# Kernel optimization log

Measured on AMD Instinct MI355X. Metric: run time of the kernel, lower is better.

## Reference

```python
import jax, jax.numpy as jnp
import numpy as np

D_MODEL = 192
D_STATE = 64
D_CONV = 4
EXPAND = 2
HEADDIM = 64
CHUNK = 256
D_INNER = EXPAND * D_MODEL            # 384
NHEADS = D_INNER // HEADDIM           # 6
CONV_DIM = D_INNER + 2 * D_STATE      # 512 (ngroups=1)
D_IN_PROJ = 2 * D_INNER + 2 * D_STATE + NHEADS  # 902


def setup_inputs() -> dict:
    key = jax.random.key(0)
    ks = jax.random.split(key, 10)
    B, H, W = 8, 64, 64
    rn = lambda k, s, sc: jax.random.normal(k, s, jnp.float32) * sc
    return {
        "x": rn(ks[0], (B, D_MODEL, H, W), 1.0),
        "norm1_w": jnp.ones((D_MODEL,), jnp.float32),
        "norm1_b": jnp.zeros((D_MODEL,), jnp.float32),
        "in_proj_w": rn(ks[1], (D_IN_PROJ, D_MODEL), D_MODEL ** -0.5),
        "conv_w": rn(ks[2], (CONV_DIM, D_CONV), D_CONV ** -0.5),
        "conv_b": jnp.zeros((CONV_DIM,), jnp.float32),
        "dt_bias": jnp.log(jnp.expm1(jax.random.uniform(ks[3], (NHEADS,), jnp.float32, 0.001, 0.1))),
        "A_log": jnp.log(jax.random.uniform(ks[4], (NHEADS,), jnp.float32, 1.0, 16.0)),
        "D_skip": jnp.ones((NHEADS,), jnp.float32),
        "ssm_norm_w": jnp.ones((D_INNER,), jnp.float32),
        "out_proj_w": rn(ks[5], (D_MODEL, D_INNER), D_INNER ** -0.5),
        "norm2_w": jnp.ones((D_MODEL,), jnp.float32),
        "norm2_b": jnp.zeros((D_MODEL,), jnp.float32),
        "ffn_w1": rn(ks[6], (2 * D_MODEL, D_MODEL), D_MODEL ** -0.5),
        "ffn_b1": jnp.zeros((2 * D_MODEL,), jnp.float32),
        "ffn_w2": rn(ks[7], (D_MODEL, 2 * D_MODEL), (2 * D_MODEL) ** -0.5),
        "ffn_b2": jnp.zeros((D_MODEL,), jnp.float32),
    }


def _layernorm(x, w, b, eps=1e-5):
    mu = jnp.mean(x, -1, keepdims=True)
    var = jnp.mean((x - mu) ** 2, -1, keepdims=True)
    return (x - mu) * jax.lax.rsqrt(var + eps) * w + b


def _segsum(a):
    # a: (..., T) -> lower-triangular segment sums, -inf above diagonal
    T = a.shape[-1]
    cs = jnp.cumsum(a, -1)
    d = cs[..., :, None] - cs[..., None, :]
    mask = jnp.tril(jnp.ones((T, T), bool))
    return jnp.where(mask, d, -jnp.inf)


def _ssd(x, A, Bm, Cm):
    # chunked SSD (Mamba2 ssd_minimal). x:(b,l,h,p) pre-scaled by dt; A:(b,l,h)=dt*A_h; Bm,Cm:(b,l,h,n)
    b, l, h, p = x.shape
    c = l // CHUNK
    x = x.reshape(b, c, CHUNK, h, p)
    A = A.reshape(b, c, CHUNK, h).transpose(0, 3, 1, 2)          # (b,h,c,t)
    Bm = Bm.reshape(b, c, CHUNK, h, D_STATE)
    Cm = Cm.reshape(b, c, CHUNK, h, D_STATE)
    A_cs = jnp.cumsum(A, -1)                                      # (b,h,c,t)
    L = jnp.exp(_segsum(A))                                       # (b,h,c,t,t)
    Y_diag = jnp.einsum('bclhn,bcshn,bhcls,bcshp->bclhp', Cm, Bm, L, x)
    decay_states = jnp.exp(A_cs[..., -1:] - A_cs)                 # (b,h,c,t)
    states = jnp.einsum('bclhn,bhcl,bclhp->bchpn', Bm, decay_states, x)
    A_last = jnp.pad(A_cs[..., -1], ((0, 0), (0, 0), (1, 0)))     # (b,h,c+1)
    decay_chunk = jnp.exp(_segsum(A_last))                        # (b,h,c+1,c+1)
    states = jnp.concatenate([jnp.zeros_like(states[:, :1]), states], axis=1)
    new_states = jnp.einsum('bhzc,bchpn->bzhpn', decay_chunk, states)
    states = new_states[:, :-1]                                   # (b,c,h,p,n) inter-chunk init states
    Y_off = jnp.einsum('bclhn,bchpn,bhcl->bclhp', Cm, states, jnp.exp(A_cs))
    return (Y_diag + Y_off).reshape(b, l, h, p)


def _mamba2(u, in_proj_w, conv_w, conv_b, dt_bias, A_log, D_skip, ssm_norm_w, out_proj_w):
    # u: (b, L, d_model) -> (b, L, d_model)
    b, l, _ = u.shape
    zxbcdt = u @ in_proj_w.T                                      # (b,l,902)
    z = zxbcdt[..., :D_INNER]
    xBC = zxbcdt[..., D_INNER:D_INNER + CONV_DIM]
    dt = jax.nn.softplus(zxbcdt[..., -NHEADS:] + dt_bias)         # (b,l,h)
    # causal depthwise conv over sequence
    xBC_t = jax.lax.conv_general_dilated(
        xBC.transpose(0, 2, 1), conv_w[:, None, :], (1,), [(D_CONV - 1, 0)],
        feature_group_count=CONV_DIM, dimension_numbers=('NCH', 'OIH', 'NCH'))
    xBC = jax.nn.silu(xBC_t.transpose(0, 2, 1) + conv_b)
    xs = xBC[..., :D_INNER].reshape(b, l, NHEADS, HEADDIM)
    Bm = jnp.broadcast_to(xBC[..., D_INNER:D_INNER + D_STATE][:, :, None, :], (b, l, NHEADS, D_STATE))
    Cm = jnp.broadcast_to(xBC[..., D_INNER + D_STATE:][:, :, None, :], (b, l, NHEADS, D_STATE))
    A = -jnp.exp(A_log)                                           # (h,)
    y = _ssd(xs * dt[..., None], dt * A, Bm, Cm)
    y = y + xs * D_skip[None, None, :, None]
    y = y.reshape(b, l, D_INNER)
    g = y * jax.nn.silu(z)                                        # gated RMSNorm
    g = g * jax.lax.rsqrt(jnp.mean(g * g, -1, keepdims=True) + 1e-5) * ssm_norm_w
    return g @ out_proj_w.T


def reference(x, norm1_w, norm1_b, in_proj_w, conv_w, conv_b, dt_bias, A_log, D_skip,
              ssm_norm_w, out_proj_w, norm2_w, norm2_b, ffn_w1, ffn_b1, ffn_w2, ffn_b2):
    B, C, H, W = x.shape
    x_flat = x.transpose(0, 2, 3, 1).reshape(B, H * W, C)
    h1 = _layernorm(x_flat, norm1_w, norm1_b)
    # faithful to source: raw reshape (B,HW,C)->(B,C,H,W), then mixer flattens to (B,L,C)
    u = h1.reshape(B, C, H, W).reshape(B, C, H * W).transpose(0, 2, 1)
    m = _mamba2(u, in_proj_w, conv_w, conv_b, dt_bias, A_log, D_skip, ssm_norm_w, out_proj_w)
    m_flat = m.transpose(0, 2, 1).reshape(B, C, H, W).transpose(0, 2, 3, 1).reshape(B, H * W, C)
    x_flat = x_flat + m_flat
    h2 = _layernorm(x_flat, norm2_w, norm2_b)
    f = jax.nn.gelu(h2 @ ffn_w1.T + ffn_b1, approximate=False) @ ffn_w2.T + ffn_b2
    x_flat = x_flat + f
    return x_flat.reshape(B, H, W, C).transpose(0, 3, 1, 2)
```

## Files before the change

### kernel.cpp

```cpp
#include <hip/hip_runtime.h>
#include <hip/hip_bf16.h>

#define BATCH 8
#define CHN   192
#define LEN   4096
#define DI    384
#define NHEAD 6
#define DST   64
#define NCHK  16

typedef __attribute__((ext_vector_type(8))) short short8;
typedef __attribute__((ext_vector_type(4))) short short4v;
typedef __attribute__((ext_vector_type(4))) float f32x4;

__device__ __forceinline__ short f2b(float f) {
  unsigned u = __builtin_bit_cast(unsigned, f);
  unsigned r = (u + 0x7FFFu + ((u >> 16) & 1u)) >> 16;
  return (short)r;
}
__device__ __forceinline__ float bf2f(short s) {
  unsigned u = ((unsigned)(unsigned short)s) << 16;
  return __builtin_bit_cast(float, u);
}

__global__ __launch_bounds__(256) void k_ln1(const float* __restrict__ x,
    const float* __restrict__ w, const float* __restrict__ b, float* __restrict__ h1) {
  __shared__ float s[192][33];
  __shared__ float red[2][32][8];
  __shared__ float mu_s[32], rs_s[32];
  int bb = blockIdx.y;
  int t0 = blockIdx.x * 32;
  int tid = threadIdx.x;
  for (int i = 0; i < 24; ++i) {
    int idx = tid + i * 256;
    int c = idx >> 5, tt = idx & 31;
    s[c][tt] = x[((size_t)bb * CHN + c) * LEN + t0 + tt];
  }
  __syncthreads();
  int tok = tid & 31, part = tid >> 5;
  float sum = 0.f, sq = 0.f;
  for (int c = part * 24; c < part * 24 + 24; ++c) { float v = s[c][tok]; sum += v; sq += v * v; }
  red[0][tok][part] = sum; red[1][tok][part] = sq;
  __syncthreads();
  if (tid < 32) {
    float su = 0.f, qq = 0.f;
    for (int p = 0; p < 8; ++p) { su += red[0][tid][p]; qq += red[1][tid][p]; }
    float mu = su / 192.f;
    float var = qq / 192.f - mu * mu;
    mu_s[tid] = mu; rs_s[tid] = rsqrtf(var + 1e-5f);
  }
  __syncthreads();
  for (int i = 0; i < 24; ++i) {
    int idx = tid + i * 256;
    int c = idx % 192, tt = idx / 192;
    float v = (s[c][tt] - mu_s[tt]) * rs_s[tt] * w[c] + b[c];
    h1[((size_t)bb * LEN + t0 + tt) * CHN + c] = v;
  }
}

__global__ void k_make_u(const float* __restrict__ h1, short* __restrict__ Ub) {
  __shared__ float s[32][33];
  int bb = blockIdx.z;
  int c0 = blockIdx.y * 32;
  int l0 = blockIdx.x * 32;
  int tx = threadIdx.x, ty = threadIdx.y;
  const float* src = h1 + (size_t)bb * (CHN * LEN);
  for (int i = 0; i < 4; ++i)
    s[ty + i * 8][tx] = src[(size_t)(c0 + ty + i * 8) * LEN + l0 + tx];
  __syncthreads();
  short* dstb = Ub + (size_t)bb * (CHN * LEN);
  for (int i = 0; i < 4; ++i)
    dstb[(size_t)(l0 + ty + i * 8) * CHN + c0 + tx] = f2b(s[tx][ty + i * 8]);
}

template <int EPI, int ABF16, int OBF16>
__global__ __launch_bounds__(256) void gemm_mfma(const void* __restrict__ Av,
    const float* __restrict__ W, const float* __restrict__ bias,
    void* __restrict__ Cv, int M, int N, int K, int ldc,
    const float* __restrict__ resid, float* __restrict__ outT) {
  __shared__ short Al[128 * 64];
  __shared__ short Wl[64 * 64];
  int m0 = blockIdx.y * 128, n0 = blockIdx.x * 64;
  int tid = threadIdx.x;
  int lane = tid & 63, wv = tid >> 6;
  int wm = (wv >> 1) * 64, wn = (wv & 1) * 32;
  int l15 = lane & 15, l4 = lane >> 4;
  f32x4 acc[4][2] = {};

  int ra = tid >> 1, ca = (tid & 1) * 32;
  int rw = tid >> 2, cw = (tid & 3) * 16;
  char* ArowL = (char*)Al + ra * 128;
  char* WrowL = (char*)Wl + rw * 128;
  int rxa = (ra & 7) << 4, rxw = (rw & 7) << 4;

  for (int k0 = 0; k0 < K; k0 += 64) {
    if (ABF16) {
      const short* Ag = (const short*)Av + (size_t)(m0 + ra) * K + k0 + ca;
#pragma unroll
      for (int q = 0; q < 4; ++q) {
        short8 pk = *(const short8*)(Ag + q * 8);
        *(short8*)(ArowL + (((ca + q * 8) * 2) ^ rxa)) = pk;
      }
    } else {
      const float* Ag = (const float*)Av + (size_t)(m0 + ra) * K + k0 + ca;
#pragma unroll
      for (int q = 0; q < 4; ++q) {
        float4 v0 = *(const float4*)(Ag + q * 8);
        float4 v1 = *(const float4*)(Ag + q * 8 + 4);
        short8 pk;
        pk[0] = f2b(v0.x); pk[1] = f2b(v0.y); pk[2] = f2b(v0.z); pk[3] = f2b(v0.w);
        pk[4] = f2b(v1.x); pk[5] = f2b(v1.y); pk[6] = f2b(v1.z); pk[7] = f2b(v1.w);
        *(short8*)(ArowL + (((ca + q * 8) * 2) ^ rxa)) = pk;
      }
    }
    {
      const float* Wg = W + (size_t)(n0 + rw) * K + k0 + cw;
#pragma unroll
      for (int q = 0; q < 2; ++q) {
        float4 v0 = *(const float4*)(Wg + q * 8);
        float4 v1 = *(const float4*)(Wg + q * 8 + 4);
        short8 pk;
        pk[0] = f2b(v0.x); pk[1] = f2b(v0.y); pk[2] = f2b(v0.z); pk[3] = f2b(v0.w);
        pk[4] = f2b(v1.x); pk[5] = f2b(v1.y); pk[6] = f2b(v1.z); pk[7] = f2b(v1.w);
        *(short8*)(WrowL + (((cw + q * 8) * 2) ^ rxw)) = pk;
      }
    }
    __syncthreads();
#pragma unroll
    for (int ks = 0; ks < 64; ks += 32) {
      short8 af[4], wf[2];
#pragma unroll
      for (int mf = 0; mf < 4; ++mf) {
        int rr = wm + mf * 16 + l15;
        af[mf] = *(const short8*)((const char*)Al + rr * 128 +
                                  (((ks + l4 * 8) * 2) ^ ((rr & 7) << 4)));
      }
#pragma unroll
      for (int nf = 0; nf < 2; ++nf) {
        int rr = wn + nf * 16 + l15;
        wf[nf] = *(const short8*)((const char*)Wl + rr * 128 +
                                  (((ks + l4 * 8) * 2) ^ ((rr & 7) << 4)));
      }
#pragma unroll
      for (int mf = 0; mf < 4; ++mf)
#pragma unroll
        for (int nf = 0; nf < 2; ++nf)
          acc[mf][nf] = __builtin_amdgcn_mfma_f32_16x16x32_bf16(
              af[mf], wf[nf], acc[mf][nf], 0, 0, 0);
    }
    __syncthreads();
  }
#pragma unroll
  for (int mf = 0; mf < 4; ++mf) {
#pragma unroll
    for (int nf = 0; nf < 2; ++nf) {
      int col = n0 + wn + nf * 16 + l15;
      float bv = (EPI >= 1 && EPI <= 3) ? bias[col] : 0.f;
      if (EPI == 3) {
        int row0 = m0 + wm + mf * 16 + l4 * 4;
        float4 o;
#pragma unroll
        for (int reg = 0; reg < 4; ++reg) {
          int row = row0 + reg;
          ((float*)&o)[reg] = acc[mf][nf][reg] + bv + resid[(size_t)row * CHN + col];
        }
        int bb_l = row0 >> 12, row_l = row0 & 4095;
        *(float4*)&outT[((size_t)bb_l * CHN + col) * LEN + row_l] = o;
      } else if (EPI == 4) {
        int row0 = m0 + wm + mf * 16 + l4 * 4;
        int bb_l = row0 >> 12, row_l = row0 & 4095;
        float4 xv = *(const float4*)&resid[((size_t)bb_l * CHN + col) * LEN + row_l];
#pragma unroll
        for (int reg = 0; reg < 4; ++reg)
          ((float*)Cv)[(size_t)(row0 + reg) * ldc + col] =
              acc[mf][nf][reg] + ((const float*)&xv)[reg];
      } else {
#pragma unroll
        for (int reg = 0; reg < 4; ++reg) {
          int row = m0 + wm + mf * 16 + l4 * 4 + reg;
          float v = acc[mf][nf][reg];
          if (EPI >= 1) v += bv;
          if (EPI == 1) v = 0.5f * v * (1.f + erff(v * 0.70710678118f));
          if (OBF16) ((short*)Cv)[(size_t)row * ldc + col] = f2b(v);
          else       ((float*)Cv)[(size_t)row * ldc + col] = v;
        }
      }
    }
  }
}

__global__ __launch_bounds__(256) void k_dt2(const float* __restrict__ h1,
    const float* __restrict__ win, const float* __restrict__ dt_bias,
    float* __restrict__ dtb) {
  __shared__ float Ut[192][65];
  __shared__ float Wl[6][192];
  int l0 = blockIdx.x * 64, bb = blockIdx.y;
  int tid = threadIdx.x;
  for (int i = tid; i < 6 * 192; i += 256)
    Wl[i / 192][i % 192] = win[(size_t)(896 + i / 192) * 192 + (i % 192)];
  const float* src = h1 + (size_t)bb * (CHN * LEN);
  for (int i = tid; i < 192 * 16; i += 256) {
    int c = i >> 4, q = i & 15;
    float4 v = *(const float4*)&src[(size_t)c * LEN + l0 + q * 4];
    *(float4*)&Ut[c][q * 4] = v;
  }
  __syncthreads();
  int tok = tid & 63, grp = tid >> 6;
  for (int h = grp; h < 6; h += 4) {
    float acc = dt_bias[h];
    for (int c = 0; c < 192; ++c) acc += Ut[c][tok] * Wl[h][c];
    dtb[((size_t)bb * LEN + l0 + tok) * NHEAD + h] =
        (acc > 20.f) ? acc : log1pf(expf(acc));
  }
}

__global__ __launch_bounds__(256) void k_conv(const short* __restrict__ zxs,
    const float* __restrict__ cw, const float* __restrict__ cb,
    short* __restrict__ xbcs) {
  __shared__ float S[67][132];
  int l0 = blockIdx.x * 64, ct = blockIdx.y, bb = blockIdx.z;
  int tid = threadIdx.x;
  int c = (tid & 31) * 4;
  int chb = ct * 128 + c;
  float wr[4][4];
#pragma unroll
  for (int j = 0; j < 4; ++j) {
    float4 w4 = *(const float4*)&cw[(size_t)(chb + j) * 4];
    wr[j][0] = w4.x; wr[j][1] = w4.y; wr[j][2] = w4.z; wr[j][3] = w4.w;
  }
  float4 bc4 = *(const float4*)&cb[chb];
  for (int idx = tid; idx < 67 * 16; idx += 256) {
    int r = idx >> 4, c8 = (idx & 15) * 8;
    int tok = l0 + r - 3;
    if (tok >= 0) {
      short8 v = *(const short8*)&zxs[((size_t)bb * LEN + tok) * 896 + 384 + ct * 128 + c8];
#pragma unroll
      for (int j = 0; j < 8; ++j) S[r][c8 + j] = bf2f(v[j]);
    } else {
#pragma unroll
      for (int j = 0; j < 8; ++j) S[r][c8 + j] = 0.f;
    }
  }
  __syncthreads();
  int t0l = tid >> 5;
#pragma unroll
  for (int it = 0; it < 8; ++it) {
    int tl = it * 8 + t0l;
    float a0 = bc4.x, a1 = bc4.y, a2 = bc4.z, a3 = bc4.w;
#pragma unroll
    for (int k = 0; k < 4; ++k) {
      float4 v = *(const float4*)&S[tl + k][c];
      a0 += v.x * wr[0][k];
      a1 += v.y * wr[1][k];
      a2 += v.z * wr[2][k];
      a3 += v.w * wr[3][k];
    }
    short4v o;
    o[0] = f2b(a0 / (1.f + __expf(-a0)));
    o[1] = f2b(a1 / (1.f + __expf(-a1)));
    o[2] = f2b(a2 / (1.f + __expf(-a2)));
    o[3] = f2b(a3 / (1.f + __expf(-a3)));
    *(short4v*)&xbcs[((size_t)bb * LEN + l0 + tl) * 512 + chb] = o;
  }
}

__global__ __launch_bounds__(256) void k_cumsum(const float* __restrict__ dtb,
    const float* __restrict__ A_log, float* __restrict__ sAg) {
  int cch = blockIdx.x, bb = blockIdx.y;
  int lane = threadIdx.x & 63, wv = threadIdx.x >> 6;
  size_t rowbase = (size_t)bb * LEN + cch * 256;
  for (int h = wv; h < NHEAD; h += 4) {
    float Ah = -expf(A_log[h]);
    float v[4];
#pragma unroll
    for (int i = 0; i < 4; ++i)
      v[i] = dtb[(rowbase + lane * 4 + i) * NHEAD + h] * Ah;
    v[1] += v[0]; v[2] += v[1]; v[3] += v[2];
    float tot = v[3];
    float sc = tot;
    for (int off = 1; off < 64; off <<= 1) {
      float o = __shfl_up(sc, off);
      if (lane >= off) sc += o;
    }
    float excl = sc - tot;
#pragma unroll
    for (int i = 0; i < 4; ++i)
      sAg[(rowbase + lane * 4 + i) * NHEAD + h] = v[i] + excl;
  }
}

__global__ __launch_bounds__(256) void k_xt(const short* __restrict__ xbcs,
    const float* __restrict__ dtb, const float* __restrict__ sAg,
    short* __restrict__ XT, short* __restrict__ XE, short* __restrict__ BtG) {
  int cch = blockIdx.x, h = blockIdx.y, bb = blockIdx.z;
  int tid = threadIdx.x;
  __shared__ float sD[256], sEl[256];
  __shared__ float T[64][68];
  size_t rowbase = (size_t)bb * LEN + cch * 256;
  sD[tid] = dtb[(rowbase + tid) * NHEAD + h];
  {
    float a = sAg[(rowbase + tid) * NHEAD + h];
    float atot = sAg[(rowbase + 255) * NHEAD + h];
    sEl[tid] = __expf(atot - a);
  }
  size_t base_xh = (((size_t)bb * NHEAD + h) * NCHK + cch) * 16384;
  size_t base_bc = ((size_t)bb * NCHK + cch) * 16384;
  int r = tid >> 2, cq = (tid & 3) * 16;
  int p = tid >> 2, sq = tid & 3;
  for (int ts = 0; ts < 4; ++ts) {
    __syncthreads();
#pragma unroll
    for (int q = 0; q < 2; ++q) {
      short8 v = *(const short8*)&xbcs[(rowbase + ts * 64 + r) * 512 + h * 64 + cq + q * 8];
#pragma unroll
      for (int j = 0; j < 8; ++j) T[r][cq + q * 8 + j] = bf2f(v[j]);
    }
    __syncthreads();
    {
      short8 x0, x1, e0, e1;
#pragma unroll
      for (int j = 0; j < 8; ++j) {
        int sl = sq * 16 + j;
        float f = T[sl][p] * sD[ts * 64 + sl];
        x0[j] = f2b(f);
        e0[j] = f2b(f * sEl[ts * 64 + sl]);
      }
#pragma unroll
      for (int j = 0; j < 8; ++j) {
        int sl = sq * 16 + 8 + j;
        float f = T[sl][p] * sD[ts * 64 + sl];
        x1[j] = f2b(f);
        e1[j] = f2b(f * sEl[ts * 64 + sl]);
      }
      size_t o = base_xh + (size_t)p * 256 + ts * 64 + sq * 16;
      *(short8*)&XT[o] = x0; *(short8*)&XT[o + 8] = x1;
      *(short8*)&XE[o] = e0; *(short8*)&XE[o + 8] = e1;
    }
    if (h == 0) {
      __syncthreads();
#pragma unroll
      for (int q = 0; q < 2; ++q) {
        short8 bv = *(const short8*)&xbcs[(rowbase + ts * 64 + r) * 512 + 384 + cq + q * 8];
#pragma unroll
        for (int j = 0; j < 8; ++j) T[r][cq + q * 8 + j] = bf2f(bv[j]);
      }
      __syncthreads();
      short8 b0, b1;
#pragma unroll
      for (int j = 0; j < 8; ++j) b0[j] = f2b(T[sq * 16 + j][p]);
#pragma unroll
      for (int j = 0; j < 8; ++j) b1[j] = f2b(T[sq * 16 + 8 + j][p]);
      size_t o = base_bc + (size_t)p * 256 + ts * 64 + sq * 16;
      *(short8*)&BtG[o] = b0; *(short8*)&BtG[o + 8] = b1;
    }
  }
}

__global__ __launch_bounds__(256) void k_states(const short* __restrict__ XE,
    const short* __restrict__ BtG, float* __restrict__ states) {
  int cch = blockIdx.x, h = blockIdx.y, bb = blockIdx.z;
  int tid = threadIdx.x;
  int lane = tid & 63, wv = tid >> 6;
  int l15 = lane & 15, l4 = lane >> 4;
  size_t base_bc = ((size_t)bb * NCHK + cch) * 16384;
  size_t base_xh = (((size_t)bb * NHEAD + h) * NCHK + cch) * 16384;
  f32x4 stacc[4] = {};
#pragma unroll
  for (int ks = 0; ks < 8; ++ks) {
    short8 aE = *(const short8*)&XE[base_xh +
        (size_t)(wv * 16 + l15) * 256 + ks * 32 + l4 * 8];
#pragma unroll
    for (int ni = 0; ni < 4; ++ni) {
      short8 bB = *(const short8*)&BtG[base_bc +
          (size_t)(ni * 16 + l15) * 256 + ks * 32 + l4 * 8];
      stacc[ni] = __builtin_amdgcn_mfma_f32_16x16x32_bf16(aE, bB, stacc[ni], 0, 0, 0);
    }
  }
  size_t stbase = (((size_t)bb * NCHK + cch) * NHEAD + h) * 4096;
#pragma unroll
  for (int ni = 0; ni < 4; ++ni)
#pragma unroll
    for (int reg = 0; reg < 4; ++reg)
      states[stbase + (size_t)(wv * 16 + l4 * 4 + reg) * 64 + ni * 16 + l15] =
          stacc[ni][reg];
}

__global__ void k_scan(const float* __restrict__ states, const float* __restrict__ sAg,
                       short* __restrict__ SinB) {
  int h = blockIdx.x, bb = blockIdx.y;
  int t = threadIdx.x;
  float S[16];
#pragma unroll
  for (int i = 0; i < 16; ++i) S[i] = 0.f;
  for (int z = 0; z < NCHK; ++z) {
    size_t base = (((size_t)bb * NCHK + z) * NHEAD + h) * 4096 + t * 16;
#pragma unroll
    for (int i = 0; i < 16; ++i) SinB[base + i] = f2b(S[i]);
    float az = __expf(sAg[((size_t)bb * LEN + z * 256 + 255) * NHEAD + h]);
#pragma unroll
    for (int i = 0; i < 16; ++i) S[i] = S[i] * az + states[base + i];
  }
}

__global__ __launch_bounds__(256) void k_ssdY(const short* __restrict__ xbcs,
    const short* __restrict__ XT, const short* __restrict__ SinB,
    const float* __restrict__ sAg, short* __restrict__ ybs) {
  int cch = blockIdx.x, h = blockIdx.y, bb = blockIdx.z;
  int tid = threadIdx.x;
  int lane = tid & 63, wv = tid >> 6;
  int l15 = lane & 15, l4 = lane >> 4;
  __shared__ float sA[256];
  __shared__ float sEt[256];
  __shared__ short St[4][64 * 64];
  size_t rowbase = (size_t)bb * LEN + cch * 256;
  {
    float av = sAg[(rowbase + tid) * NHEAD + h];
    sA[tid] = av;
    sEt[tid] = __expf(av);
  }
  __syncthreads();
  size_t base_xh = (((size_t)bb * NHEAD + h) * NCHK + cch) * 16384;
  size_t base_s = (((size_t)bb * NCHK + cch) * NHEAD + h) * 4096;
  int tp = wv;
  short* Sw = St[wv];
  short8 cf[4][2];
#pragma unroll
  for (int ni = 0; ni < 4; ++ni)
#pragma unroll
    for (int ks = 0; ks < 2; ++ks)
      cf[ni][ks] = *(const short8*)&xbcs[(rowbase + tp * 64 + ni * 16 + l15) * 512 +
                                         448 + ks * 32 + l4 * 8];
  float At[4];
#pragma unroll
  for (int ni = 0; ni < 4; ++ni) At[ni] = sA[tp * 64 + ni * 16 + l15];

  f32x4 yacc[4][4];
#pragma unroll
  for (int mi = 0; mi < 4; ++mi) {
    f32x4 yo[4] = {};
#pragma unroll
    for (int ks = 0; ks < 2; ++ks) {
      short8 aS = *(const short8*)&SinB[base_s +
          (size_t)(mi * 16 + l15) * 64 + ks * 32 + l4 * 8];
#pragma unroll
      for (int ni = 0; ni < 4; ++ni)
        yo[ni] = __builtin_amdgcn_mfma_f32_16x16x32_bf16(aS, cf[ni][ks], yo[ni], 0, 0, 0);
    }
#pragma unroll
    for (int ni = 0; ni < 4; ++ni) {
      float et = sEt[tp * 64 + ni * 16 + l15];
#pragma unroll
      for (int reg = 0; reg < 4; ++reg) yacc[mi][ni][reg] = et * yo[ni][reg];
    }
  }
  for (int st = 0; st <= tp; ++st) {
    bool diag = (st == tp);
#pragma unroll
    for (int mi = 0; mi < 4; ++mi) {
      const short* brow = &xbcs[(rowbase + st * 64 + mi * 16 + l15) * 512 + 384 + l4 * 8];
      short8 af0 = *(const short8*)brow;
      short8 af1 = *(const short8*)(brow + 32);
      f32x4 s0[4];
#pragma unroll
      for (int ni = 0; ni < 4; ++ni) {
        f32x4 t = {};
        t = __builtin_amdgcn_mfma_f32_16x16x32_bf16(af0, cf[ni][0], t, 0, 0, 0);
        t = __builtin_amdgcn_mfma_f32_16x16x32_bf16(af1, cf[ni][1], t, 0, 0, 0);
        s0[ni] = t;
      }
      float As[4];
#pragma unroll
      for (int reg = 0; reg < 4; ++reg) As[reg] = sA[st * 64 + mi * 16 + l4 * 4 + reg];
      int s_loc0 = mi * 16 + l4 * 4;
#pragma unroll
      for (int ni = 0; ni < 4; ++ni) {
        int t_loc = ni * 16 + l15;
        short4v pk;
#pragma unroll
        for (int reg = 0; reg < 4; ++reg) {
          float v = __expf(At[ni] - As[reg]) * s0[ni][reg];
          if (diag && (s_loc0 + reg) > t_loc) v = 0.f;
          pk[reg] = f2b(v);
        }
        *(short4v*)((char*)Sw + t_loc * 128 +
                    (((s_loc0 * 2)) ^ ((t_loc & 7) << 4))) = pk;
      }
    }
#pragma unroll
    for (int ks = 0; ks < 2; ++ks) {
      short8 bS[4], aX[4];
#pragma unroll
      for (int ni = 0; ni < 4; ++ni) {
        int rt = ni * 16 + l15;
        bS[ni] = *(const short8*)((const char*)Sw + rt * 128 +
                                  (((ks * 32 + l4 * 8) * 2) ^ ((rt & 7) << 4)));
      }
#pragma unroll
      for (int mi = 0; mi < 4; ++mi)
        aX[mi] = *(const short8*)&XT[base_xh +
            (size_t)(mi * 16 + l15) * 256 + st * 64 + ks * 32 + l4 * 8];
#pragma unroll
      for (int mi = 0; mi < 4; ++mi)
#pragma unroll
        for (int ni = 0; ni < 4; ++ni)
          yacc[mi][ni] = __builtin_amdgcn_mfma_f32_16x16x32_bf16(
              aX[mi], bS[ni], yacc[mi][ni], 0, 0, 0);
    }
  }
#pragma unroll
  for (int ni = 0; ni < 4; ++ni) {
    int tg = tp * 64 + ni * 16 + l15;
#pragma unroll
    for (int mi = 0; mi < 4; ++mi) {
      short4v o;
#pragma unroll
      for (int reg = 0; reg < 4; ++reg) o[reg] = f2b(yacc[mi][ni][reg]);
      *(short4v*)&ybs[(rowbase + tg) * DI + h * 64 + mi * 16 + l4 * 4] = o;
    }
  }
}

__global__ __launch_bounds__(128) void k_gate(const short* __restrict__ ybs,
    const short* __restrict__ zxs, const short* __restrict__ xbcs,
    const float* __restrict__ Dsk, const float* __restrict__ nw,
    short* __restrict__ gn) {
  int row = blockIdx.x;
  int tid = threadIdx.x;
  float g[3]; float sq = 0.f;
#pragma unroll
  for (int i = 0; i < 3; ++i) {
    int d = tid + i * 128;
    int h = d >> 6;
    float z = bf2f(zxs[(size_t)row * 896 + d]);
    float yy = bf2f(ybs[(size_t)row * DI + d]) +
               Dsk[h] * bf2f(xbcs[(size_t)row * 512 + d]);
    float gg = yy * (z / (1.f + expf(-z)));
    g[i] = gg; sq += gg * gg;
  }
  for (int off = 32; off > 0; off >>= 1) sq += __shfl_down(sq, off);
  __shared__ float wsum[2];
  if ((tid & 63) == 0) wsum[tid >> 6] = sq;
  __syncthreads();
  float rs = rsqrtf((wsum[0] + wsum[1]) / 384.f + 1e-5f);
#pragma unroll
  for (int i = 0; i < 3; ++i) {
    int d = tid + i * 128;
    gn[(size_t)row * DI + d] = f2b(g[i] * rs * nw[d]);
  }
}

__global__ __launch_bounds__(64) void k_ln2(const float* __restrict__ r,
    const float* __restrict__ w, const float* __restrict__ b, short* __restrict__ h2) {
  int row = blockIdx.x;
  int tid = threadIdx.x;
  float v[3]; float sum = 0.f;
#pragma unroll
  for (int i = 0; i < 3; ++i) { v[i] = r[(size_t)row * CHN + tid + i * 64]; sum += v[i]; }
  for (int off = 32; off > 0; off >>= 1) sum += __shfl_down(sum, off);
  sum = __shfl(sum, 0);
  float mu = sum / 192.f;
  float sq = 0.f;
#pragma unroll
  for (int i = 0; i < 3; ++i) { float d = v[i] - mu; sq += d * d; }
  for (int off = 32; off > 0; off >>= 1) sq += __shfl_down(sq, off);
  sq = __shfl(sq, 0);
  float rs = rsqrtf(sq / 192.f + 1e-5f);
#pragma unroll
  for (int i = 0; i < 3; ++i) {
    int c = tid + i * 64;
    h2[(size_t)row * CHN + c] = f2b((v[i] - mu) * rs * w[c] + b[c]);
  }
}

extern "C" void kernel_launch(void* const* d_in, const int* in_sizes, int n_in,
                              void* d_out, int out_size, void* d_ws, size_t ws_size,
                              hipStream_t stream) {
  const float* x     = (const float*)d_in[0];
  const float* n1w   = (const float*)d_in[1];
  const float* n1b   = (const float*)d_in[2];
  const float* win   = (const float*)d_in[3];
  const float* cw    = (const float*)d_in[4];
  const float* cb    = (const float*)d_in[5];
  const float* dtbw  = (const float*)d_in[6];
  const float* alog  = (const float*)d_in[7];
  const float* dskip = (const float*)d_in[8];
  const float* snw   = (const float*)d_in[9];
  const float* wout  = (const float*)d_in[10];
  const float* n2w   = (const float*)d_in[11];
  const float* n2b   = (const float*)d_in[12];
  const float* w1    = (const float*)d_in[13];
  const float* b1    = (const float*)d_in[14];
  const float* w2    = (const float*)d_in[15];
  const float* b2    = (const float*)d_in[16];
  float* out = (float*)d_out;

  int g = 8;
  size_t G192, S_ZXH, S_DT, S_XBCH, S_ST;
  for (;;) {
    G192   = (size_t)g * LEN * CHN;
    S_ZXH  = (size_t)g * LEN * 448;
    S_DT   = (size_t)g * LEN * NHEAD;
    S_XBCH = (size_t)g * LEN * 256;
    S_ST   = (size_t)g * NCHK * NHEAD * 4096;
    size_t TOTAL = 2 * G192 + S_ZXH + 2 * S_DT + S_XBCH + G192 / 2 +
                   2 * G192 + (size_t)g * 131072 + S_ST + S_ST / 2 + 64;
    if (TOTAL * 4 <= ws_size) break;
    if (g == 1) return;
    g >>= 1;
  }

  float* ws   = (float*)d_ws;
  float* h1   = ws;
  short* ybs  = (short*)ws;
  short* zxs  = (short*)(ws + 2 * G192);
  float* dtb  = ws + 2 * G192 + S_ZXH;
  float* sag  = dtb + S_DT;
  float* xbp  = sag + S_DT;
  short* xbcs = (short*)xbp;
  short* f1s  = (short*)xbp;
  float* up   = xbp + S_XBCH;
  short* Ubf  = (short*)up;
  short* h2s  = (short*)up;
  float* xtp  = up + G192 / 2;
  short* XT   = (short*)xtp;
  short* gns  = (short*)xtp;
  float* xep  = xtp + G192;
  short* XE   = (short*)xep;
  float* resid= xep;
  float* btp  = xep + G192;
  short* BtG  = (short*)btp;
  float* st   = btp + (size_t)g * 131072;
  short* SinB = (short*)(st + S_ST);

  const int M = g * LEN;

  for (int b0 = 0; b0 < BATCH; b0 += g) {
    const float* xg  = x   + (size_t)b0 * CHN * LEN;
    float*       og  = out + (size_t)b0 * CHN * LEN;

    k_ln1<<<dim3(LEN / 32, g), 256, 0, stream>>>(xg, n1w, n1b, h1);
    k_make_u<<<dim3(LEN / 32, CHN / 32, g), dim3(32, 8), 0, stream>>>(h1, Ubf);
    gemm_mfma<0, 1, 1><<<dim3(896 / 64, M / 128), 256, 0, stream>>>(
        Ubf, win, nullptr, zxs, M, 896, CHN, 896, nullptr, nullptr);
    k_dt2<<<dim3(LEN / 64, g), 256, 0, stream>>>(h1, win, dtbw, dtb);
    k_conv<<<dim3(LEN / 64, 4, g), 256, 0, stream>>>(zxs, cw, cb, xbcs);
    k_cumsum<<<dim3(NCHK, g), 256, 0, stream>>>(dtb, alog, sag);
    k_xt<<<dim3(NCHK, NHEAD, g), 256, 0, stream>>>(xbcs, dtb, sag, XT, XE, BtG);
    k_states<<<dim3(NCHK, NHEAD, g), 256, 0, stream>>>(XE, BtG, st);
    k_scan<<<dim3(NHEAD, g), 256, 0, stream>>>(st, sag, SinB);
    k_ssdY<<<dim3(NCHK, NHEAD, g), 256, 0, stream>>>(xbcs, XT, SinB, sag, ybs);
    k_gate<<<dim3(M), 128, 0, stream>>>(ybs, zxs, xbcs, dskip, snw, gns);
    gemm_mfma<4, 1, 0><<<dim3(CHN / 64, M / 128), 256, 0, stream>>>(
        gns, wout, nullptr, resid, M, CHN, DI, CHN, xg, nullptr);
    k_ln2<<<dim3(M), 64, 0, stream>>>(resid, n2w, n2b, h2s);
    gemm_mfma<1, 1, 1><<<dim3(DI / 64, M / 128), 256, 0, stream>>>(
        h2s, w1, b1, f1s, M, DI, CHN, DI, nullptr, nullptr);
    gemm_mfma<3, 1, 0><<<dim3(CHN / 64, M / 128), 256, 0, stream>>>(
        f1s, w2, b2, nullptr, M, CHN, DI, CHN, resid, og);
  }
}
```

Before: 269.1 us.

## Split SSD output kernel into one-wavefront blocks per 64-row subchunk

The intra-chunk SSD output kernel used 256-thread blocks where each wavefront handled one 64-row subchunk, with a causal triangle making wave work uneven (1 to 4 inner iterations). Now each block is a single wavefront covering one subchunk, launched on a grid four times larger, so finished waves release resources right away instead of waiting for the slowest wave in the block. The exp of the cumulative decay is computed in registers instead of being staged in shared memory. In exchange, every block reloads the full 256-entry decay vector, and there are more small blocks to schedule.

```diff
diff --git a/kernel.cpp b/kernel.cpp
--- a/kernel.cpp
+++ b/kernel.cpp
@@ -402,27 +402,21 @@
   }
 }
 
-__global__ __launch_bounds__(256) void k_ssdY(const short* __restrict__ xbcs,
+__global__ __launch_bounds__(64) void k_ssdY(const short* __restrict__ xbcs,
     const short* __restrict__ XT, const short* __restrict__ SinB,
     const float* __restrict__ sAg, short* __restrict__ ybs) {
-  int cch = blockIdx.x, h = blockIdx.y, bb = blockIdx.z;
-  int tid = threadIdx.x;
-  int lane = tid & 63, wv = tid >> 6;
+  int q = blockIdx.x;
+  int cch = q >> 2, tp = q & 3;
+  int h = blockIdx.y, bb = blockIdx.z;
+  int lane = threadIdx.x;
   int l15 = lane & 15, l4 = lane >> 4;
   __shared__ float sA[256];
-  __shared__ float sEt[256];
-  __shared__ short St[4][64 * 64];
+  __shared__ short St[64 * 64];
   size_t rowbase = (size_t)bb * LEN + cch * 256;
-  {
-    float av = sAg[(rowbase + tid) * NHEAD + h];
-    sA[tid] = av;
-    sEt[tid] = __expf(av);
-  }
-  __syncthreads();
+  for (int i = lane; i < 256; i += 64)
+    sA[i] = sAg[(rowbase + i) * NHEAD + h];
   size_t base_xh = (((size_t)bb * NHEAD + h) * NCHK + cch) * 16384;
   size_t base_s = (((size_t)bb * NCHK + cch) * NHEAD + h) * 4096;
-  int tp = wv;
-  short* Sw = St[wv];
   short8 cf[4][2];
 #pragma unroll
   for (int ni = 0; ni < 4; ++ni)
@@ -430,9 +424,12 @@
     for (int ks = 0; ks < 2; ++ks)
       cf[ni][ks] = *(const short8*)&xbcs[(rowbase + tp * 64 + ni * 16 + l15) * 512 +
                                          448 + ks * 32 + l4 * 8];
-  float At[4];
-#pragma unroll
-  for (int ni = 0; ni < 4; ++ni) At[ni] = sA[tp * 64 + ni * 16 + l15];
+  float At[4], Et[4];
+#pragma unroll
+  for (int ni = 0; ni < 4; ++ni) {
+    At[ni] = sA[tp * 64 + ni * 16 + l15];
+    Et[ni] = __expf(At[ni]);
+  }
 
   f32x4 yacc[4][4];
 #pragma unroll
@@ -447,11 +444,9 @@
         yo[ni] = __builtin_amdgcn_mfma_f32_16x16x32_bf16(aS, cf[ni][ks], yo[ni], 0, 0, 0);
     }
 #pragma unroll
-    for (int ni = 0; ni < 4; ++ni) {
-      float et = sEt[tp * 64 + ni * 16 + l15];
-#pragma unroll
-      for (int reg = 0; reg < 4; ++reg) yacc[mi][ni][reg] = et * yo[ni][reg];
-    }
+    for (int ni = 0; ni < 4; ++ni)
+#pragma unroll
+      for (int reg = 0; reg < 4; ++reg) yacc[mi][ni][reg] = Et[ni] * yo[ni][reg];
   }
   for (int st = 0; st <= tp; ++st) {
     bool diag = (st == tp);
@@ -482,7 +477,7 @@
           if (diag && (s_loc0 + reg) > t_loc) v = 0.f;
           pk[reg] = f2b(v);
         }
-        *(short4v*)((char*)Sw + t_loc * 128 +
+        *(short4v*)((char*)St + t_loc * 128 +
                     (((s_loc0 * 2)) ^ ((t_loc & 7) << 4))) = pk;
       }
     }
@@ -492,7 +487,7 @@
 #pragma unroll
       for (int ni = 0; ni < 4; ++ni) {
         int rt = ni * 16 + l15;
-        bS[ni] = *(const short8*)((const char*)Sw + rt * 128 +
+        bS[ni] = *(const short8*)((const char*)St + rt * 128 +
                                   (((ks * 32 + l4 * 8) * 2) ^ ((rt & 7) << 4)));
       }
 #pragma unroll
@@ -648,7 +643,7 @@
     k_xt<<<dim3(NCHK, NHEAD, g), 256, 0, stream>>>(xbcs, dtb, sag, XT, XE, BtG);
     k_states<<<dim3(NCHK, NHEAD, g), 256, 0, stream>>>(XE, BtG, st);
     k_scan<<<dim3(NHEAD, g), 256, 0, stream>>>(st, sag, SinB);
-    k_ssdY<<<dim3(NCHK, NHEAD, g), 256, 0, stream>>>(xbcs, XT, SinB, sag, ybs);
+    k_ssdY<<<dim3(NCHK * 4, NHEAD, g), 64, 0, stream>>>(xbcs, XT, SinB, sag, ybs);
     k_gate<<<dim3(M), 128, 0, stream>>>(ybs, zxs, xbcs, dskip, snw, gns);
     gemm_mfma<4, 1, 0><<<dim3(CHN / 64, M / 128), 256, 0, stream>>>(
         gns, wout, nullptr, resid, M, CHN, DI, CHN, xg, nullptr);
```

Result: slower. 278.3 us (+3.4%).

## Fuse chunk-state MFMA into k_xt via swizzled LDS tiles, drop XE/BtG buffers

Applied to the files above, without the earlier changes.

The k_states kernel is folded into k_xt. The dt- and decay-scaled X tile and the transposed B tile are now staged in XOR-swizzled shared memory, and the per-chunk state MFMA accumulates there one 64-step slice at a time. This removes the global XE and BtG buffers, their writes and reads, and one kernel launch. In exchange, every head block now transposes B itself (previously only h==0 did), adds two syncthreads per slice, and uses more LDS.

```diff
diff --git a/kernel.cpp b/kernel.cpp
--- a/kernel.cpp
+++ b/kernel.cpp
@@ -291,11 +291,15 @@
 
 __global__ __launch_bounds__(256) void k_xt(const short* __restrict__ xbcs,
     const float* __restrict__ dtb, const float* __restrict__ sAg,
-    short* __restrict__ XT, short* __restrict__ XE, short* __restrict__ BtG) {
+    short* __restrict__ XT, float* __restrict__ states) {
   int cch = blockIdx.x, h = blockIdx.y, bb = blockIdx.z;
   int tid = threadIdx.x;
+  int lane = tid & 63, wv = tid >> 6;
+  int l15 = lane & 15, l4 = lane >> 4;
   __shared__ float sD[256], sEl[256];
   __shared__ float T[64][68];
+  __shared__ short XEl[64 * 64];
+  __shared__ short BTl[64 * 64];
   size_t rowbase = (size_t)bb * LEN + cch * 256;
   sD[tid] = dtb[(rowbase + tid) * NHEAD + h];
   {
@@ -304,9 +308,10 @@
     sEl[tid] = __expf(atot - a);
   }
   size_t base_xh = (((size_t)bb * NHEAD + h) * NCHK + cch) * 16384;
-  size_t base_bc = ((size_t)bb * NCHK + cch) * 16384;
   int r = tid >> 2, cq = (tid & 3) * 16;
   int p = tid >> 2, sq = tid & 3;
+  int pswz = (p & 7) << 4;
+  f32x4 stacc[4] = {};
   for (int ts = 0; ts < 4; ++ts) {
     __syncthreads();
 #pragma unroll
@@ -334,46 +339,39 @@
       }
       size_t o = base_xh + (size_t)p * 256 + ts * 64 + sq * 16;
       *(short8*)&XT[o] = x0; *(short8*)&XT[o + 8] = x1;
-      *(short8*)&XE[o] = e0; *(short8*)&XE[o + 8] = e1;
-    }
-    if (h == 0) {
-      __syncthreads();
-#pragma unroll
-      for (int q = 0; q < 2; ++q) {
-        short8 bv = *(const short8*)&xbcs[(rowbase + ts * 64 + r) * 512 + 384 + cq + q * 8];
-#pragma unroll
-        for (int j = 0; j < 8; ++j) T[r][cq + q * 8 + j] = bf2f(bv[j]);
-      }
-      __syncthreads();
+      *(short8*)((char*)XEl + p * 128 + ((sq * 32) ^ pswz)) = e0;
+      *(short8*)((char*)XEl + p * 128 + ((sq * 32 + 16) ^ pswz)) = e1;
+    }
+    __syncthreads();
+#pragma unroll
+    for (int q = 0; q < 2; ++q) {
+      short8 bv = *(const short8*)&xbcs[(rowbase + ts * 64 + r) * 512 + 384 + cq + q * 8];
+#pragma unroll
+      for (int j = 0; j < 8; ++j) T[r][cq + q * 8 + j] = bf2f(bv[j]);
+    }
+    __syncthreads();
+    {
       short8 b0, b1;
 #pragma unroll
       for (int j = 0; j < 8; ++j) b0[j] = f2b(T[sq * 16 + j][p]);
 #pragma unroll
       for (int j = 0; j < 8; ++j) b1[j] = f2b(T[sq * 16 + 8 + j][p]);
-      size_t o = base_bc + (size_t)p * 256 + ts * 64 + sq * 16;
-      *(short8*)&BtG[o] = b0; *(short8*)&BtG[o + 8] = b1;
-    }
-  }
-}
-
-__global__ __launch_bounds__(256) void k_states(const short* __restrict__ XE,
-    const short* __restrict__ BtG, float* __restrict__ states) {
-  int cch = blockIdx.x, h = blockIdx.y, bb = blockIdx.z;
-  int tid = threadIdx.x;
-  int lane = tid & 63, wv = tid >> 6;
-  int l15 = lane & 15, l4 = lane >> 4;
-  size_t base_bc = ((size_t)bb * NCHK + cch) * 16384;
-  size_t base_xh = (((size_t)bb * NHEAD + h) * NCHK + cch) * 16384;
-  f32x4 stacc[4] = {};
-#pragma unroll
-  for (int ks = 0; ks < 8; ++ks) {
-    short8 aE = *(const short8*)&XE[base_xh +
-        (size_t)(wv * 16 + l15) * 256 + ks * 32 + l4 * 8];
-#pragma unroll
-    for (int ni = 0; ni < 4; ++ni) {
-      short8 bB = *(const short8*)&BtG[base_bc +
-          (size_t)(ni * 16 + l15) * 256 + ks * 32 + l4 * 8];
-      stacc[ni] = __builtin_amdgcn_mfma_f32_16x16x32_bf16(aE, bB, stacc[ni], 0, 0, 0);
+      *(short8*)((char*)BTl + p * 128 + ((sq * 32) ^ pswz)) = b0;
+      *(short8*)((char*)BTl + p * 128 + ((sq * 32 + 16) ^ pswz)) = b1;
+    }
+    __syncthreads();
+#pragma unroll
+    for (int ks = 0; ks < 2; ++ks) {
+      int rp = wv * 16 + l15;
+      short8 aE = *(const short8*)((const char*)XEl + rp * 128 +
+                                   (((ks * 32 + l4 * 8) * 2) ^ ((rp & 7) << 4)));
+#pragma unroll
+      for (int ni = 0; ni < 4; ++ni) {
+        int rn = ni * 16 + l15;
+        short8 bB = *(const short8*)((const char*)BTl + rn * 128 +
+                                     (((ks * 32 + l4 * 8) * 2) ^ ((rn & 7) << 4)));
+        stacc[ni] = __builtin_amdgcn_mfma_f32_16x16x32_bf16(aE, bB, stacc[ni], 0, 0, 0);
+      }
     }
   }
   size_t stbase = (((size_t)bb * NCHK + cch) * NHEAD + h) * 4096;
@@ -603,7 +601,7 @@
     S_XBCH = (size_t)g * LEN * 256;
     S_ST   = (size_t)g * NCHK * NHEAD * 4096;
     size_t TOTAL = 2 * G192 + S_ZXH + 2 * S_DT + S_XBCH + G192 / 2 +
-                   2 * G192 + (size_t)g * 131072 + S_ST + S_ST / 2 + 64;
+                   2 * G192 + S_ST + S_ST / 2 + 64;
     if (TOTAL * 4 <= ws_size) break;
     if (g == 1) return;
     g >>= 1;
@@ -625,11 +623,8 @@
   short* XT   = (short*)xtp;
   short* gns  = (short*)xtp;
   float* xep  = xtp + G192;
-  short* XE   = (short*)xep;
   float* resid= xep;
-  float* btp  = xep + G192;
-  short* BtG  = (short*)btp;
-  float* st   = btp + (size_t)g * 131072;
+  float* st   = xep + G192;
   short* SinB = (short*)(st + S_ST);
 
   const int M = g * LEN;
@@ -645,8 +640,7 @@
     k_dt2<<<dim3(LEN / 64, g), 256, 0, stream>>>(h1, win, dtbw, dtb);
     k_conv<<<dim3(LEN / 64, 4, g), 256, 0, stream>>>(zxs, cw, cb, xbcs);
     k_cumsum<<<dim3(NCHK, g), 256, 0, stream>>>(dtb, alog, sag);
-    k_xt<<<dim3(NCHK, NHEAD, g), 256, 0, stream>>>(xbcs, dtb, sag, XT, XE, BtG);
-    k_states<<<dim3(NCHK, NHEAD, g), 256, 0, stream>>>(XE, BtG, st);
+    k_xt<<<dim3(NCHK, NHEAD, g), 256, 0, stream>>>(xbcs, dtb, sag, XT, st);
     k_scan<<<dim3(NHEAD, g), 256, 0, stream>>>(st, sag, SinB);
     k_ssdY<<<dim3(NCHK, NHEAD, g), 256, 0, stream>>>(xbcs, XT, SinB, sag, ybs);
     k_gate<<<dim3(M), 128, 0, stream>>>(ybs, zxs, xbcs, dskip, snw, gns);
```

Result: faster. 252.0 us (-6.4%).
